# Kernel optimization log

Hardware: AMD Instinct MI355X
Metric: run time of the kernel (lower is better)

## Reference

```python
import jax, jax.numpy as jnp
import numpy as np

B, N = 4, 4096


def setup_inputs() -> dict:
    key = jax.random.key(0)
    k1, k2, k3, k4 = jax.random.split(key, 4)
    xyz1 = jax.random.normal(k1, (B, N, 3), dtype=jnp.float32)
    xyz2 = jax.random.normal(k2, (B, N, 3), dtype=jnp.float32)
    nor1 = jax.random.normal(k3, (B, N, 3), dtype=jnp.float32)
    nor2 = jax.random.normal(k4, (B, N, 3), dtype=jnp.float32)
    return {"xyz1": xyz1, "xyz2": xyz2, "nor1": nor1, "nor2": nor2}


def _kernel_sum(xa, xb, na, nb):
    # sum_{i,j} exp(-||xa_i - xb_j||^2) * (na_i . nb_j)^2
    diff = xa[:, :, None, :] - xb[:, None, :, :]          # [B, Na, Nb, 3]
    S = jnp.sum(diff * diff, axis=-1)                      # squared distances
    D = jnp.einsum('bid,bjd->bij', na, nb)                 # normal dot products
    return jnp.sum(jnp.exp(-S) * (D * D))


def reference(xyz1, xyz2, nor1, nor2):
    kxx = _kernel_sum(xyz1, xyz1, nor1, nor1)
    kyy = _kernel_sum(xyz2, xyz2, nor2, nor2)
    kxy = _kernel_sum(xyz1, xyz2, nor1, nor2)
    return kxx + kyy - 2.0 * kxy
```

## Files before the change

kernel.cpp:

```cpp
#include <hip/hip_runtime.h>


typedef short bf16x8 __attribute__((ext_vector_type(8)));
typedef float f32x16 __attribute__((ext_vector_type(16)));
typedef float f32x2  __attribute__((ext_vector_type(2)));

#define NPTS 4096
#define BATCH 4
#define JCHUNK 512
#define LOG2E 1.4426950408889634f

#define NDIAG (2 * BATCH * 8 * 2)
#define NOFF  (2 * BATCH * 28 * 4)
#define NXY   (BATCH * 32 * 8)
#define GRID_MAIN (NDIAG + NOFF + NXY)

#define RSTRIDE 65536
#define REG(side, form, mat, b) \
    (((((((side)*2 + (form))*2 + (mat))*BATCH) + (b))) * (size_t)RSTRIDE)
#define PARTIALS_OFF (32 * (size_t)RSTRIDE)

__constant__ unsigned char OFF_TBL[28] = {
    0x01,0x02,0x03,0x04,0x05,0x06,0x07,
    0x12,0x13,0x14,0x15,0x16,0x17,
    0x23,0x24,0x25,0x26,0x27,
    0x34,0x35,0x36,0x37,
    0x45,0x46,0x47,
    0x56,0x57,
    0x67
};

static __device__ __forceinline__ short f2bf(float f) {
    unsigned u = __builtin_bit_cast(unsigned, f);
    unsigned r = u + 0x7fffu + ((u >> 16) & 1u);
    return (short)(r >> 16);
}
static __device__ __forceinline__ void split(float v, float& h, float& l) {
    unsigned u = __builtin_bit_cast(unsigned, v);
    unsigned rb = (u + 0x7fffu + ((u >> 16) & 1u)) & 0xffff0000u;
    h = __builtin_bit_cast(float, rb);
    l = v - h;
}

static __device__ __forceinline__ void encodeA(float x0, float x1, float x2,
                                               float n0, float n1, float n2,
                                               float fS[16], float fD[16]) {
    float s2 = fmaf(x2, x2, fmaf(x1, x1, x0 * x0));
    float gh, gl; split(-LOG2E * s2, gh, gl);
    float u0h,u0l,u1h,u1l,u2h,u2l;
    split(2.f*LOG2E*x0, u0h, u0l);
    split(2.f*LOG2E*x1, u1h, u1l);
    split(2.f*LOG2E*x2, u2h, u2l);
    fS[0]=gh;  fS[1]=gl;  fS[2]=1.f; fS[3]=1.f;
    fS[4]=u0h; fS[5]=u0h; fS[6]=u0l;
    fS[7]=u1h; fS[8]=u1h; fS[9]=u1l;
    fS[10]=u2h; fS[11]=u2h; fS[12]=u2l;
    fS[13]=0.f; fS[14]=0.f; fS[15]=0.f;
    float m0h,m0l,m1h,m1l,m2h,m2l;
    split(n0, m0h, m0l); split(n1, m1h, m1l); split(n2, m2h, m2l);
    fD[0]=m0h; fD[1]=m0h; fD[2]=m0l;
    fD[3]=m1h; fD[4]=m1h; fD[5]=m1l;
    fD[6]=m2h; fD[7]=m2h; fD[8]=m2l;
#pragma unroll
    for (int k = 9; k < 16; ++k) fD[k] = 0.f;
}

static __device__ __forceinline__ void encodeB(float x0, float x1, float x2,
                                               float n0, float n1, float n2,
                                               float fS[16], float fD[16]) {
    float s2 = fmaf(x2, x2, fmaf(x1, x1, x0 * x0));
    float gh, gl; split(-LOG2E * s2, gh, gl);
    float v0h,v0l,v1h,v1l,v2h,v2l;
    split(x0, v0h, v0l); split(x1, v1h, v1l); split(x2, v2h, v2l);
    fS[0]=1.f; fS[1]=1.f; fS[2]=gh;  fS[3]=gl;
    fS[4]=v0h; fS[5]=v0l; fS[6]=v0h;
    fS[7]=v1h; fS[8]=v1l; fS[9]=v1h;
    fS[10]=v2h; fS[11]=v2l; fS[12]=v2h;
    fS[13]=0.f; fS[14]=0.f; fS[15]=0.f;
    float m0h,m0l,m1h,m1l,m2h,m2l;
    split(n0, m0h, m0l); split(n1, m1h, m1l); split(n2, m2h, m2l);
    fD[0]=m0h; fD[1]=m0l; fD[2]=m0h;
    fD[3]=m1h; fD[4]=m1l; fD[5]=m1h;
    fD[6]=m2h; fD[7]=m2l; fD[8]=m2h;
#pragma unroll
    for (int k = 9; k < 16; ++k) fD[k] = 0.f;
}

static __device__ __forceinline__ void store_units(short* base, int u0, const float f[16]) {
    bf16x8 a, b;
#pragma unroll
    for (int k = 0; k < 8; ++k) { a[k] = f2bf(f[k]); b[k] = f2bf(f[k + 8]); }
    *(bf16x8*)&base[(size_t)u0 * 8] = a;
    *(bf16x8*)&base[((size_t)u0 + 32) * 8] = b;
}

__global__ __launch_bounds__(256)
void vf_encode(const float* __restrict__ xyz1, const float* __restrict__ xyz2,
               const float* __restrict__ nor1, const float* __restrict__ nor2,
               short* __restrict__ ws)
{
    int gid = blockIdx.x * 256 + threadIdx.x;
    int side = gid >> 14;
    int b    = (gid >> 12) & 3;
    int j    = gid & 4095;

    const float* px = side ? xyz2 : xyz1;
    const float* pn = side ? nor2 : nor1;
    size_t off = ((size_t)b * NPTS + j) * 3;
    float x0 = px[off], x1 = px[off+1], x2 = px[off+2];
    float n0 = pn[off], n1 = pn[off+1], n2 = pn[off+2];

    float fS[16], fD[16];
    int u0 = (j >> 5) * 64 + (j & 31);

    encodeA(x0, x1, x2, n0, n1, n2, fS, fD);
    store_units(ws + REG(side, 0, 0, b), u0, fS);
    store_units(ws + REG(side, 0, 1, b), u0, fD);
    encodeB(x0, x1, x2, n0, n1, n2, fS, fD);
    store_units(ws + REG(side, 1, 0, b), u0, fS);
    store_units(ws + REG(side, 1, 1, b), u0, fD);
}

static __device__ __forceinline__ void epi(const f32x16& aS, const f32x16& aD,
                                           f32x2& q0, f32x2& q1) {
#pragma unroll
    for (int e = 0; e < 16; e += 4) {
        f32x2 ex0, ex1, d0, d1;
        ex0[0] = __builtin_amdgcn_exp2f(aS[e+0]);
        ex0[1] = __builtin_amdgcn_exp2f(aS[e+1]);
        ex1[0] = __builtin_amdgcn_exp2f(aS[e+2]);
        ex1[1] = __builtin_amdgcn_exp2f(aS[e+3]);
        d0[0] = aD[e+0]; d0[1] = aD[e+1];
        d1[0] = aD[e+2]; d1[1] = aD[e+3];
        q0 = __builtin_elementwise_fma(ex0 * d0, d0, q0);
        q1 = __builtin_elementwise_fma(ex1 * d1, d1, q1);
    }
}

__global__ __launch_bounds__(256, 4)
void vf_main(short* __restrict__ ws)
{
    __shared__ short sBS[JCHUNK * 16];
    __shared__ short sBD[JCHUNK * 16];

    int blk = blockIdx.x;
    const int tid  = threadIdx.x;
    const int lane = tid & 63;
    const int wv   = tid >> 6;

    int term, b, jc;
    int isdiag = 0;
    int ib = 0;
    int g = 0, job = 0;
    float wgt = 0.f;

    if (blk < NDIAG) {
        isdiag = 1;
        int d = blk;
        term = d >> 6; d &= 63;
        b = d & 3; d >>= 2;
        g = d & 7; job = d >> 3;
        jc = g;
    } else if (blk < NDIAG + NOFF) {
        int o = blk - NDIAG;
        term = (o < NOFF / 2) ? 0 : 1;
        if (term) o -= NOFF / 2;
        b = o & 3; o >>= 2;
        int sub = o & 3; int st = o >> 2;
        unsigned e = OFF_TBL[st];
        ib = (e >> 4) * 4 + sub;
        jc = e & 15;
        wgt = 2.f;
    } else {
        int x = blk - (NDIAG + NOFF);
        term = 2;
        b = x & 3; x >>= 2;
        ib = x & 31;
        jc = x >> 5;
        wgt = -2.f;
    }

    int sideA = (term == 1) ? 1 : 0;
    int sideB = (term == 0) ? 0 : 1;

    const short* aSp = ws + REG(sideA, 0, 0, b);
    const short* aDp = ws + REG(sideA, 0, 1, b);
    const short* bSp = ws + REG(sideB, 1, 0, b) + (size_t)jc * 1024 * 8;
    const short* bDp = ws + REG(sideB, 1, 1, b) + (size_t)jc * 1024 * 8;

#pragma unroll
    for (int k = 0; k < 4; ++k) {
        int ul = tid + k * 256;
        *(bf16x8*)&sBS[(size_t)ul * 8] = *(const bf16x8*)&bSp[(size_t)ul * 8];
        *(bf16x8*)&sBD[(size_t)ul * 8] = *(const bf16x8*)&bDp[(size_t)ul * 8];
    }

    f32x16 z;
#pragma unroll
    for (int k = 0; k < 16; ++k) z[k] = 0.f;

    f32x2 q0 = {0.f, 0.f}, q1 = {0.f, 0.f};
    f32x2 p0 = {0.f, 0.f}, p1 = {0.f, 0.f};
    float part;

    if (!isdiag) {
        int ua = (ib * 4 + wv) * 64 + lane;
        bf16x8 AS = *(const bf16x8*)&aSp[(size_t)ua * 8];
        bf16x8 AD = *(const bf16x8*)&aDp[(size_t)ua * 8];

        __syncthreads();

#pragma unroll
        for (int jt = 0; jt < JCHUNK / 32; ++jt) {
            int u = (jt * 64 + lane) * 8;
            bf16x8 BS = *(const bf16x8*)&sBS[u];
            bf16x8 BD = *(const bf16x8*)&sBD[u];
            f32x16 aSacc = __builtin_amdgcn_mfma_f32_32x32x16_bf16(AS, BS, z, 0, 0, 0);
            f32x16 aDacc = __builtin_amdgcn_mfma_f32_32x32x16_bf16(AD, BD, z, 0, 0, 0);
            epi(aSacc, aDacc, q0, q1);
        }
        part = wgt * ((q0[0] + q0[1]) + (q1[0] + q1[1]));
    } else {
        int r   = job * 4 + wv;
        int rt1 = r, rt2 = 15 - r;
        int ua1 = (g * 16 + rt1) * 64 + lane;
        int ua2 = (g * 16 + rt2) * 64 + lane;
        bf16x8 AS1 = *(const bf16x8*)&aSp[(size_t)ua1 * 8];
        bf16x8 AD1 = *(const bf16x8*)&aDp[(size_t)ua1 * 8];
        bf16x8 AS2 = *(const bf16x8*)&aSp[(size_t)ua2 * 8];
        bf16x8 AD2 = *(const bf16x8*)&aDp[(size_t)ua2 * 8];

        __syncthreads();

#pragma unroll
        for (int jt = 0; jt < JCHUNK / 32; ++jt) {
            int u = (jt * 64 + lane) * 8;
            bf16x8 BS = *(const bf16x8*)&sBS[u];
            bf16x8 BD = *(const bf16x8*)&sBD[u];
            if (jt >= rt1) {
                f32x16 aS = __builtin_amdgcn_mfma_f32_32x32x16_bf16(AS1, BS, z, 0, 0, 0);
                f32x16 aD = __builtin_amdgcn_mfma_f32_32x32x16_bf16(AD1, BD, z, 0, 0, 0);
                if (jt == rt1) epi(aS, aD, p0, p1);
                else           epi(aS, aD, q0, q1);
            }
            if (jt >= rt2) {
                f32x16 aS = __builtin_amdgcn_mfma_f32_32x32x16_bf16(AS2, BS, z, 0, 0, 0);
                f32x16 aD = __builtin_amdgcn_mfma_f32_32x32x16_bf16(AD2, BD, z, 0, 0, 0);
                if (jt == rt2) epi(aS, aD, p0, p1);
                else           epi(aS, aD, q0, q1);
            }
        }
        part = ((p0[0] + p0[1]) + (p1[0] + p1[1]))
             + 2.f * ((q0[0] + q0[1]) + (q1[0] + q1[1]));
    }

#pragma unroll
    for (int off = 32; off > 0; off >>= 1)
        part += __shfl_down(part, off, 64);

    __syncthreads();
    float* red = (float*)sBS;
    if (lane == 0) red[wv] = part;
    __syncthreads();
    if (tid == 0) {
        float s = (red[0] + red[1]) + (red[2] + red[3]);
        float* partials = (float*)(ws + PARTIALS_OFF);
        partials[blk] = s;
    }
}

__global__ __launch_bounds__(256)
void vf_reduce(const short* __restrict__ ws, float* __restrict__ out)
{
    const float* partials = (const float*)(ws + PARTIALS_OFF);
    int tid = threadIdx.x;
    double s = 0.0;
#pragma unroll
    for (int k = 0; k < (GRID_MAIN + 255) / 256; ++k) {
        int idx = tid + k * 256;
        if (idx < GRID_MAIN) s += (double)partials[idx];
    }
#pragma unroll
    for (int off = 32; off > 0; off >>= 1)
        s += __shfl_down(s, off, 64);
    __shared__ double red[4];
    int lane = tid & 63, wv = tid >> 6;
    if (lane == 0) red[wv] = s;
    __syncthreads();
    if (tid == 0)
        out[0] = (float)((red[0] + red[1]) + (red[2] + red[3]));
}

extern "C" void kernel_launch(void* const* d_in, const int* in_sizes, int n_in,
                              void* d_out, int out_size, void* d_ws, size_t ws_size,
                              hipStream_t stream) {
    const float* xyz1 = (const float*)d_in[0];
    const float* xyz2 = (const float*)d_in[1];
    const float* nor1 = (const float*)d_in[2];
    const float* nor2 = (const float*)d_in[3];
    float* out = (float*)d_out;
    short* ws  = (short*)d_ws;

    vf_encode<<<(2 * BATCH * NPTS) / 256, 256, 0, stream>>>(xyz1, xyz2, nor1, nor2, ws);
    vf_main<<<GRID_MAIN, 256, 0, stream>>>(ws);
    vf_reduce<<<1, 256, 0, stream>>>(ws, out);
}
```

Before: 81.64 us.

## Fuse bf16 encoding into main kernel and drop separate encode pass

Removes the standalone encode kernel and its workspace round trip. Each block now encodes its B-chunk directly into shared memory and encodes its A-row fragments in registers from the raw float inputs. This saves a kernel launch and global write/read traffic, at the cost of recomputing encodings redundantly across blocks and adding ALU work and uncoalesced stride-3 float loads before the MFMA loop.

```diff
diff --git a/kernel.cpp b/kernel.cpp
--- a/kernel.cpp
+++ b/kernel.cpp
@@ -14,11 +14,6 @@
 #define NOFF  (2 * BATCH * 28 * 4)
 #define NXY   (BATCH * 32 * 8)
 #define GRID_MAIN (NDIAG + NOFF + NXY)
-
-#define RSTRIDE 65536
-#define REG(side, form, mat, b) \
-    (((((((side)*2 + (form))*2 + (mat))*BATCH) + (b))) * (size_t)RSTRIDE)
-#define PARTIALS_OFF (32 * (size_t)RSTRIDE)
 
 __constant__ unsigned char OFF_TBL[28] = {
     0x01,0x02,0x03,0x04,0x05,0x06,0x07,
@@ -86,39 +81,9 @@
     for (int k = 9; k < 16; ++k) fD[k] = 0.f;
 }
 
-static __device__ __forceinline__ void store_units(short* base, int u0, const float f[16]) {
-    bf16x8 a, b;
-#pragma unroll
-    for (int k = 0; k < 8; ++k) { a[k] = f2bf(f[k]); b[k] = f2bf(f[k + 8]); }
-    *(bf16x8*)&base[(size_t)u0 * 8] = a;
-    *(bf16x8*)&base[((size_t)u0 + 32) * 8] = b;
-}
-
-__global__ __launch_bounds__(256)
-void vf_encode(const float* __restrict__ xyz1, const float* __restrict__ xyz2,
-               const float* __restrict__ nor1, const float* __restrict__ nor2,
-               short* __restrict__ ws)
-{
-    int gid = blockIdx.x * 256 + threadIdx.x;
-    int side = gid >> 14;
-    int b    = (gid >> 12) & 3;
-    int j    = gid & 4095;
-
-    const float* px = side ? xyz2 : xyz1;
-    const float* pn = side ? nor2 : nor1;
-    size_t off = ((size_t)b * NPTS + j) * 3;
-    float x0 = px[off], x1 = px[off+1], x2 = px[off+2];
-    float n0 = pn[off], n1 = pn[off+1], n2 = pn[off+2];
-
-    float fS[16], fD[16];
-    int u0 = (j >> 5) * 64 + (j & 31);
-
-    encodeA(x0, x1, x2, n0, n1, n2, fS, fD);
-    store_units(ws + REG(side, 0, 0, b), u0, fS);
-    store_units(ws + REG(side, 0, 1, b), u0, fD);
-    encodeB(x0, x1, x2, n0, n1, n2, fS, fD);
-    store_units(ws + REG(side, 1, 0, b), u0, fS);
-    store_units(ws + REG(side, 1, 1, b), u0, fD);
+static __device__ __forceinline__ void pack2(const float f[16], bf16x8& lo, bf16x8& hi) {
+#pragma unroll
+    for (int k = 0; k < 8; ++k) { lo[k] = f2bf(f[k]); hi[k] = f2bf(f[k + 8]); }
 }
 
 static __device__ __forceinline__ void epi(const f32x16& aS, const f32x16& aD,
@@ -138,7 +103,9 @@
 }
 
 __global__ __launch_bounds__(256, 4)
-void vf_main(short* __restrict__ ws)
+void vf_main(const float* __restrict__ xyz1, const float* __restrict__ xyz2,
+             const float* __restrict__ nor1, const float* __restrict__ nor2,
+             float* __restrict__ partials)
 {
     __shared__ short sBS[JCHUNK * 16];
     __shared__ short sBD[JCHUNK * 16];
@@ -183,17 +150,29 @@
     int sideA = (term == 1) ? 1 : 0;
     int sideB = (term == 0) ? 0 : 1;
 
-    const short* aSp = ws + REG(sideA, 0, 0, b);
-    const short* aDp = ws + REG(sideA, 0, 1, b);
-    const short* bSp = ws + REG(sideB, 1, 0, b) + (size_t)jc * 1024 * 8;
-    const short* bDp = ws + REG(sideB, 1, 1, b) + (size_t)jc * 1024 * 8;
-
-#pragma unroll
-    for (int k = 0; k < 4; ++k) {
-        int ul = tid + k * 256;
-        *(bf16x8*)&sBS[(size_t)ul * 8] = *(const bf16x8*)&bSp[(size_t)ul * 8];
-        *(bf16x8*)&sBD[(size_t)ul * 8] = *(const bf16x8*)&bDp[(size_t)ul * 8];
-    }
+    const float* pxA = (sideA ? xyz2 : xyz1) + (size_t)b * NPTS * 3;
+    const float* pnA = (sideA ? nor2 : nor1) + (size_t)b * NPTS * 3;
+    const float* pxB = (sideB ? xyz2 : xyz1) + (size_t)b * NPTS * 3;
+    const float* pnB = (sideB ? nor2 : nor1) + (size_t)b * NPTS * 3;
+
+#pragma unroll
+    for (int k = 0; k < 2; ++k) {
+        int q = tid + k * 256;
+        size_t off = (size_t)(jc * JCHUNK + q) * 3;
+        float fS[16], fD[16];
+        encodeB(pxB[off], pxB[off+1], pxB[off+2],
+                pnB[off], pnB[off+1], pnB[off+2], fS, fD);
+        bf16x8 slo, shi, dlo, dhi;
+        pack2(fS, slo, shi);
+        pack2(fD, dlo, dhi);
+        int u = (q >> 5) * 64 + (q & 31);
+        *(bf16x8*)&sBS[(size_t)u * 8]        = slo;
+        *(bf16x8*)&sBS[((size_t)u + 32) * 8] = shi;
+        *(bf16x8*)&sBD[(size_t)u * 8]        = dlo;
+        *(bf16x8*)&sBD[((size_t)u + 32) * 8] = dhi;
+    }
+
+    const int hi = lane >> 5;
 
     f32x16 z;
 #pragma unroll
@@ -204,9 +183,20 @@
     float part;
 
     if (!isdiag) {
-        int ua = (ib * 4 + wv) * 64 + lane;
-        bf16x8 AS = *(const bf16x8*)&aSp[(size_t)ua * 8];
-        bf16x8 AD = *(const bf16x8*)&aDp[(size_t)ua * 8];
+        int p = (ib * 4 + wv) * 32 + (lane & 31);
+        size_t offA = (size_t)p * 3;
+        float fS[16], fD[16];
+        encodeA(pxA[offA], pxA[offA+1], pxA[offA+2],
+                pnA[offA], pnA[offA+1], pnA[offA+2], fS, fD);
+        bf16x8 slo, shi, dlo, dhi;
+        pack2(fS, slo, shi);
+        pack2(fD, dlo, dhi);
+        bf16x8 AS, AD;
+#pragma unroll
+        for (int k = 0; k < 8; ++k) {
+            AS[k] = hi ? shi[k] : slo[k];
+            AD[k] = hi ? dhi[k] : dlo[k];
+        }
 
         __syncthreads();
 
@@ -223,12 +213,37 @@
     } else {
         int r   = job * 4 + wv;
         int rt1 = r, rt2 = 15 - r;
-        int ua1 = (g * 16 + rt1) * 64 + lane;
-        int ua2 = (g * 16 + rt2) * 64 + lane;
-        bf16x8 AS1 = *(const bf16x8*)&aSp[(size_t)ua1 * 8];
-        bf16x8 AD1 = *(const bf16x8*)&aDp[(size_t)ua1 * 8];
-        bf16x8 AS2 = *(const bf16x8*)&aSp[(size_t)ua2 * 8];
-        bf16x8 AD2 = *(const bf16x8*)&aDp[(size_t)ua2 * 8];
+        bf16x8 AS1, AD1, AS2, AD2;
+        {
+            int p = (g * 16 + rt1) * 32 + (lane & 31);
+            size_t offA = (size_t)p * 3;
+            float fS[16], fD[16];
+            encodeA(pxA[offA], pxA[offA+1], pxA[offA+2],
+                    pnA[offA], pnA[offA+1], pnA[offA+2], fS, fD);
+            bf16x8 slo, shi, dlo, dhi;
+            pack2(fS, slo, shi);
+            pack2(fD, dlo, dhi);
+#pragma unroll
+            for (int k = 0; k < 8; ++k) {
+                AS1[k] = hi ? shi[k] : slo[k];
+                AD1[k] = hi ? dhi[k] : dlo[k];
+            }
+        }
+        {
+            int p = (g * 16 + rt2) * 32 + (lane & 31);
+            size_t offA = (size_t)p * 3;
+            float fS[16], fD[16];
+            encodeA(pxA[offA], pxA[offA+1], pxA[offA+2],
+                    pnA[offA], pnA[offA+1], pnA[offA+2], fS, fD);
+            bf16x8 slo, shi, dlo, dhi;
+            pack2(fS, slo, shi);
+            pack2(fD, dlo, dhi);
+#pragma unroll
+            for (int k = 0; k < 8; ++k) {
+                AS2[k] = hi ? shi[k] : slo[k];
+                AD2[k] = hi ? dhi[k] : dlo[k];
+            }
+        }
 
         __syncthreads();
 
@@ -264,15 +279,13 @@
     __syncthreads();
     if (tid == 0) {
         float s = (red[0] + red[1]) + (red[2] + red[3]);
-        float* partials = (float*)(ws + PARTIALS_OFF);
         partials[blk] = s;
     }
 }
 
 __global__ __launch_bounds__(256)
-void vf_reduce(const short* __restrict__ ws, float* __restrict__ out)
+void vf_reduce(const float* __restrict__ partials, float* __restrict__ out)
 {
-    const float* partials = (const float*)(ws + PARTIALS_OFF);
     int tid = threadIdx.x;
     double s = 0.0;
 #pragma unroll
@@ -299,9 +312,8 @@
     const float* nor1 = (const float*)d_in[2];
     const float* nor2 = (const float*)d_in[3];
     float* out = (float*)d_out;
-    short* ws  = (short*)d_ws;
-
-    vf_encode<<<(2 * BATCH * NPTS) / 256, 256, 0, stream>>>(xyz1, xyz2, nor1, nor2, ws);
-    vf_main<<<GRID_MAIN, 256, 0, stream>>>(ws);
-    vf_reduce<<<1, 256, 0, stream>>>(ws, out);
-}
+    float* partials = (float*)d_ws;
+
+    vf_main<<<GRID_MAIN, 256, 0, stream>>>(xyz1, xyz2, nor1, nor2, partials);
+    vf_reduce<<<1, 256, 0, stream>>>(partials, out);
+}
```

Result: faster. 77.71 us (median of 2 runs) (-4.8%).
